# Kernel tuning notes

Hardware: AMD Instinct MI355X
Metric: run time of the kernel (lower is better)

Reference implementation:

```python
import jax, jax.numpy as jnp
import numpy as np
from jax import lax

CHANNELS, MID, GROUPS, PATCH = 512, 512, 8, 16
DROP_RATE = 0.1
NEG = -1e9


def setup_inputs() -> dict:
    key = jax.random.key(0)
    k0, k1, k2, k3, k4, k5 = jax.random.split(key, 6)
    B, T = 2, 8192
    x = jax.random.normal(k0, (B, CHANNELS, T), dtype=jnp.float32)
    # weight-norm conv is reparametrized plain conv; sample small weights directly
    W_qkv = jax.random.normal(k1, (3 * MID, CHANNELS // GROUPS, 5, 1), dtype=jnp.float32) * 0.05
    b_qkv = jax.random.normal(k2, (3 * MID,), dtype=jnp.float32) * 0.05
    W_out = jax.random.normal(k3, (CHANNELS, MID, 3), dtype=jnp.float32) * 0.05
    b_out = jax.random.normal(k4, (CHANNELS,), dtype=jnp.float32) * 0.05
    # bernoulli(p=dropRate) mask on k (detached in the original), shape of k
    drop_mask = (jax.random.uniform(k5, (B, MID, T // PATCH, PATCH)) < DROP_RATE).astype(jnp.float32)
    return {"x": x, "W_qkv": W_qkv, "b_qkv": b_qkv, "W_out": W_out, "b_out": b_out, "drop_mask": drop_mask}


def reference(x, W_qkv, b_qkv, W_out, b_out, drop_mask):
    B, C, T = x.shape
    pad = (-T) % PATCH  # static
    if pad:
        x = jnp.pad(x, ((0, 0), (0, 0), (0, pad)))
    wordNum = (T + pad) // PATCH
    x4 = x.reshape(B, C, wordNum, PATCH)  # [B,C,wordNum,patch]
    qkv = lax.conv_general_dilated(
        x4, W_qkv, window_strides=(1, 1), padding=[(2, 2), (0, 0)],
        dimension_numbers=("NCHW", "OIHW", "NCHW"), feature_group_count=GROUPS,
    ) + b_qkv[None, :, None, None]
    q, k, v = jnp.split(qkv, 3, axis=1)  # each [B,MID,wordNum,patch]
    k = k + drop_mask * NEG  # inline bernoulli dropout on k (mask is a constant)
    d = MID * PATCH

    def flat(t):  # [B,MID,wordNum,patch] -> [B,wordNum,MID*patch]
        return t.transpose(0, 2, 1, 3).reshape(B, wordNum, d)

    q = jax.nn.softmax(flat(q), axis=-1)   # softmax over features
    k = jax.nn.softmax(flat(k), axis=-2)   # softmax over sequence
    v = flat(v)
    kv = jnp.einsum("bki,bkj->bij", k, v)  # [B,d,d]
    out = jnp.einsum("bik,bkj->bij", q, kv)  # [B,wordNum,d]
    out = out.reshape(B, wordNum, MID, PATCH).transpose(0, 2, 1, 3).reshape(B, MID, wordNum * PATCH)
    out = lax.conv_general_dilated(
        out, W_out, window_strides=(1,), padding=[(1, 1)],
        dimension_numbers=("NCH", "OIH", "NCH"),
    ) + b_out[None, :, None]
    if pad:
        out = out[:, :, :-pad]
    return out
```

## Files before the change

kernel.cpp:

```cpp
#include <hip/hip_runtime.h>

#define TT 8192
#define NEGC -1000000000.0f

typedef _Float16 f16;
typedef f16 half8 __attribute__((ext_vector_type(8)));
typedef float floatx16 __attribute__((ext_vector_type(16)));

#define MFMA(a, b, c) __builtin_amdgcn_mfma_f32_32x32x16_f16(a, b, c, 0, 0, 0)

__device__ __forceinline__ half8 lds_read_frag(const f16* lds, int row, int chunk) {
    return *(const half8*)(lds + row * 64 + ((chunk ^ (row & 7)) << 3));
}
__device__ __forceinline__ void lds_write_chunk(f16* lds, int row, int chunk, half8 v) {
    *(half8*)(lds + row * 64 + ((chunk ^ (row & 7)) << 3)) = v;
}

__global__ __launch_bounds__(256) void prep_w(
    const float* __restrict__ Wq, const float* __restrict__ Wo,
    f16* __restrict__ WqP, f16* __restrict__ WoP)
{
    int i = blockIdx.x * 256 + threadIdx.x;
    const int NQ = 48 * 5 * 4 * 512;
    if (i < NQ) {
        int idx = i & 511, l = idx >> 3, e = idx & 7;
        int fi = i >> 9;
        int ks = fi & 3; fi >>= 2;
        int kh = fi % 5; int cb = fi / 5;
        int o = cb * 32 + (l & 31);
        int ci = ks * 16 + (l >> 5) * 8 + e;
        WqP[i] = (f16)Wq[o * 320 + ci * 5 + kh];
    } else {
        int j = i - NQ;
        if (j < 16 * 3 * 8 * 4 * 512) {
            int idx = j & 511, l = idx >> 3, e = idx & 7;
            int fj = j >> 9;
            int ks = fj & 3; fj >>= 2;
            int kc = fj & 7; fj >>= 3;
            int kt = fj % 3; int cb = fj / 3;
            int co = cb * 32 + (l & 31);
            int ci = kc * 64 + ks * 16 + (l >> 5) * 8 + e;
            WoP[j] = (f16)Wo[co * 1536 + ci * 3 + kt];
        }
    }
}

__global__ __launch_bounds__(256) void transpose_cvt(
    const float* __restrict__ src, size_t bstride, f16* __restrict__ dst)
{
    __shared__ float tl[64][65];
    int tid = threadIdx.x;
    int t0 = blockIdx.x * 64, c0 = blockIdx.y * 64, b = blockIdx.z;
    const float* sp = src + (size_t)b * bstride + (size_t)c0 * TT + t0;
#pragma unroll
    for (int i = 0; i < 16; i++) {
        int row = (tid >> 6) + i * 4;
        tl[row][tid & 63] = sp[(size_t)row * TT + (tid & 63)];
    }
    __syncthreads();
    f16* dp = dst + ((size_t)b * TT + t0) * 512 + c0;
#pragma unroll
    for (int i = 0; i < 16; i++) {
        int t = (tid >> 6) + i * 4;
        dp[(size_t)t * 512 + (tid & 63)] = (f16)tl[tid & 63][t];
    }
}

__global__ __launch_bounds__(256) void qkv_mfma(
    const f16* __restrict__ xT, const f16* __restrict__ WqP, const float* __restrict__ bq,
    f16* __restrict__ qk16, f16* __restrict__ vb16)
{
    __shared__ f16 xs[320 * 64];
    int tid = threadIdx.x;
    int b = blockIdx.x >> 5;
    int t0 = (blockIdx.x & 31) * 256;
    int m = blockIdx.y;
    int ob = m * 64;
    int g = m / 3;

    const f16* xb = xT + ((size_t)b * TT) * 512 + g * 64;
#pragma unroll
    for (int lp = 0; lp < 10; lp++) {
        int q = tid + lp * 256;
        int row = q >> 3, c16 = q & 7;
        int t = t0 - 32 + row;
        half8 v = {};
        if ((unsigned)t < (unsigned)TT) v = *(const half8*)(xb + (size_t)t * 512 + c16 * 8);
        lds_write_chunk(xs, row, c16, v);
    }
    __syncthreads();

    int wid = tid >> 6, l = tid & 63;
    int ln31 = l & 31, lhi = l >> 5;
    floatx16 acc[2][2] = {};
#pragma unroll
    for (int kh = 0; kh < 5; kh++) {
#pragma unroll
        for (int ks = 0; ks < 4; ks++) {
            int fi = ((m * 2) * 5 + kh) * 4 + ks;
            half8 a0 = *(const half8*)(WqP + (size_t)fi * 512 + l * 8);
            half8 a1 = *(const half8*)(WqP + (size_t)(fi + 20) * 512 + l * 8);
            int chunk = ks * 2 + lhi;
            int r0 = wid * 64 + kh * 16 + ln31;
            half8 b0 = lds_read_frag(xs, r0, chunk);
            half8 b1 = lds_read_frag(xs, r0 + 32, chunk);
            acc[0][0] = MFMA(a0, b0, acc[0][0]);
            acc[0][1] = MFMA(a0, b1, acc[0][1]);
            acc[1][0] = MFMA(a1, b0, acc[1][0]);
            acc[1][1] = MFMA(a1, b1, acc[1][1]);
        }
    }
#pragma unroll
    for (int mf = 0; mf < 2; mf++)
#pragma unroll
        for (int nf = 0; nf < 2; nf++)
#pragma unroll
            for (int r = 0; r < 16; r++) {
                int o = ob + mf * 32 + (r & 3) + 8 * (r >> 2) + 4 * lhi;
                int t = t0 + wid * 64 + nf * 32 + ln31;
                float val = acc[mf][nf][r] + bq[o];
                if (o < 1024)
                    qk16[((size_t)b * 1024 + o) * TT + t] = (f16)val;
                else
                    vb16[((size_t)b * 512 + (o - 1024)) * TT + t] = (f16)val;
            }
}

__global__ __launch_bounds__(256) void softmax_q(f16* __restrict__ qk16)
{
    int w = blockIdx.x, b = blockIdx.y, tid = threadIdx.x;
    f16* base = qk16 + (size_t)b * 1024 * TT + (size_t)w * 16;

    float val[32];
    float mx = -1e30f;
#pragma unroll
    for (int kk = 0; kk < 32; kk++) {
        int e = tid + kk * 256;
        float v = (float)base[((size_t)(e >> 4)) * TT + (e & 15)];
        val[kk] = v;
        mx = fmaxf(mx, v);
    }
#pragma unroll
    for (int o = 32; o > 0; o >>= 1) mx = fmaxf(mx, __shfl_xor(mx, o));
    __shared__ float red[4];
    int wv = tid >> 6;
    if ((tid & 63) == 0) red[wv] = mx;
    __syncthreads();
    mx = fmaxf(fmaxf(red[0], red[1]), fmaxf(red[2], red[3]));

    float s = 0.f;
#pragma unroll
    for (int kk = 0; kk < 32; kk++) { val[kk] = __expf(val[kk] - mx); s += val[kk]; }
#pragma unroll
    for (int o = 32; o > 0; o >>= 1) s += __shfl_xor(s, o);
    __syncthreads();
    if ((tid & 63) == 0) red[wv] = s;
    __syncthreads();
    s = red[0] + red[1] + red[2] + red[3];
    float inv = 1.f / s;
#pragma unroll
    for (int kk = 0; kk < 32; kk++) {
        int e = tid + kk * 256;
        base[((size_t)(e >> 4)) * TT + (e & 15)] = (f16)(val[kk] * inv);
    }
}

__global__ __launch_bounds__(256) void softmax_k(
    f16* __restrict__ qk16, const float* __restrict__ mask)
{
    int c = blockIdx.x, b = blockIdx.y, tid = threadIdx.x;
    f16* kp = qk16 + ((size_t)(b * 1024 + 512 + c)) * TT;
    const float* mp = mask + ((size_t)(b * 512 + c)) * TT;

    float val[32];
    float mx = -1e30f;
#pragma unroll
    for (int kk = 0; kk < 32; kk++) {
        int e = tid + kk * 256;
        float v = (float)kp[e] + mp[e] * NEGC;
        val[kk] = v;
        mx = fmaxf(mx, v);
    }
    mx = fmaxf(mx, __shfl_xor(mx, 16));
    mx = fmaxf(mx, __shfl_xor(mx, 32));
    __shared__ float red[4][16];
    int wv = tid >> 6, ln = tid & 63;
    if (ln < 16) red[wv][ln] = mx;
    __syncthreads();
    int p = tid & 15;
    mx = fmaxf(fmaxf(red[0][p], red[1][p]), fmaxf(red[2][p], red[3][p]));

    float s = 0.f;
#pragma unroll
    for (int kk = 0; kk < 32; kk++) { val[kk] = __expf(val[kk] - mx); s += val[kk]; }
    s += __shfl_xor(s, 16);
    s += __shfl_xor(s, 32);
    __syncthreads();
    if (ln < 16) red[wv][ln] = s;
    __syncthreads();
    s = red[0][p] + red[1][p] + red[2][p] + red[3][p];
    float inv = 1.f / s;
#pragma unroll
    for (int kk = 0; kk < 32; kk++)
        kp[tid + kk * 256] = (f16)(val[kk] * inv);
}

__global__ __launch_bounds__(256) void vperm(
    const f16* __restrict__ vb16, f16* __restrict__ vpw)
{
    int c = blockIdx.x, b = blockIdx.y, tid = threadIdx.x;
    __shared__ f16 tl[512 * 17];
    const f16* ip = vb16 + ((size_t)b * 512 + c) * TT;
    f16* op = vpw + ((size_t)b * 512 + c) * 16 * 512;
#pragma unroll
    for (int i = 0; i < 32; i++) {
        int e = tid + i * 256;
        tl[(e >> 4) * 17 + (e & 15)] = ip[e];
    }
    __syncthreads();
#pragma unroll
    for (int i = 0; i < 32; i++) {
        int o = tid + i * 256;
        op[o] = tl[(o & 511) * 17 + (o >> 9)];
    }
}

__global__ __launch_bounds__(256) void qk_mfma(
    const f16* __restrict__ qk16, float* __restrict__ Spart)
{
    __shared__ f16 As[128 * 64];
    __shared__ f16 Bs[128 * 64];
    int tid = threadIdx.x;
    int mt = blockIdx.x & 3, nt = blockIdx.x >> 2;
    int kz = blockIdx.y, b = blockIdx.z;
    int iw0 = mt * 128, w0 = nt * 128;
    const f16* qb_ = qk16 + (size_t)b * 1024 * TT;
    const f16* kb_ = qb_ + (size_t)512 * TT;
    int wid = tid >> 6, l = tid & 63, ln31 = l & 31, lhi = l >> 5;
    int wm = (wid >> 1) * 64, wn = (wid & 1) * 64;
    floatx16 acc[2][2] = {};

    for (int step = 0; step < 8; step++) {
        int c_abs = kz * 32 + step * 4 + wid;
        __syncthreads();
        const f16* qrow = qb_ + (size_t)c_abs * TT + iw0 * 16;
        const f16* krow = kb_ + (size_t)c_abs * TT + w0 * 16;
#pragma unroll
        for (int i = 0; i < 4; i++) {
            int j = l + i * 64;
            int row = j >> 1, ch = wid * 2 + (j & 1);
            lds_write_chunk(As, row, ch, *(const half8*)(qrow + j * 8));
            lds_write_chunk(Bs, row, ch, *(const half8*)(krow + j * 8));
        }
        __syncthreads();
#pragma unroll
        for (int ks = 0; ks < 4; ks++) {
            int chunk = ks * 2 + lhi;
            half8 a0 = lds_read_frag(As, wm + ln31, chunk);
            half8 a1 = lds_read_frag(As, wm + 32 + ln31, chunk);
            half8 b0 = lds_read_frag(Bs, wn + ln31, chunk);
            half8 b1 = lds_read_frag(Bs, wn + 32 + ln31, chunk);
            acc[0][0] = MFMA(a0, b0, acc[0][0]);
            acc[0][1] = MFMA(a0, b1, acc[0][1]);
            acc[1][0] = MFMA(a1, b0, acc[1][0]);
            acc[1][1] = MFMA(a1, b1, acc[1][1]);
        }
    }
    float* Sp = Spart + ((size_t)(kz * 2 + b) * 512) * 512;
#pragma unroll
    for (int mf = 0; mf < 2; mf++)
#pragma unroll
        for (int nf = 0; nf < 2; nf++)
#pragma unroll
            for (int r = 0; r < 16; r++) {
                int iw = iw0 + wm + mf * 32 + (r & 3) + 8 * (r >> 2) + 4 * lhi;
                int w = w0 + wn + nf * 32 + ln31;
                Sp[(size_t)iw * 512 + w] = acc[mf][nf][r];
            }
}

__global__ __launch_bounds__(256) void s_reduce(
    const float* __restrict__ Spart, f16* __restrict__ S16)
{
    int id = blockIdx.x * 256 + threadIdx.x;
    float s = 0.f;
#pragma unroll
    for (int kz = 0; kz < 16; kz++) s += Spart[(size_t)kz * 524288 + id];
    S16[id] = (f16)s;
}

__global__ __launch_bounds__(256) void sv_mfma(
    const f16* __restrict__ S16, const f16* __restrict__ vpw, f16* __restrict__ abufT)
{
    __shared__ f16 As[128 * 64];
    __shared__ f16 Bs[128 * 64];
    int tid = threadIdx.x;
    int mt = blockIdx.x, nt = blockIdx.y;
    int b = blockIdx.z >> 4, p = blockIdx.z & 15;
    int iw0 = mt * 128, c0n = nt * 128;
    const f16* Sb = S16 + (size_t)b * 512 * 512;
    const f16* vb_ = vpw + ((size_t)b * 512) * 16 * 512;
    int wid = tid >> 6, l = tid & 63, ln31 = l & 31, lhi = l >> 5;
    int wm = (wid >> 1) * 64, wn = (wid & 1) * 64;
    floatx16 acc[2][2] = {};

    for (int step = 0; step < 8; step++) {
        int w0k = step * 64;
        __syncthreads();
#pragma unroll
        for (int li = 0; li < 4; li++) {
            int q = tid + li * 256;
            int row = q >> 3, c16 = q & 7;
            half8 av = *(const half8*)(Sb + (size_t)(iw0 + row) * 512 + w0k + c16 * 8);
            half8 bv = *(const half8*)(vb_ + ((size_t)(c0n + row) * 16 + p) * 512 + w0k + c16 * 8);
            lds_write_chunk(As, row, c16, av);
            lds_write_chunk(Bs, row, c16, bv);
        }
        __syncthreads();
#pragma unroll
        for (int ks = 0; ks < 4; ks++) {
            int chunk = ks * 2 + lhi;
            half8 a0 = lds_read_frag(As, wm + ln31, chunk);
            half8 a1 = lds_read_frag(As, wm + 32 + ln31, chunk);
            half8 b0 = lds_read_frag(Bs, wn + ln31, chunk);
            half8 b1 = lds_read_frag(Bs, wn + 32 + ln31, chunk);
            acc[0][0] = MFMA(a0, b0, acc[0][0]);
            acc[0][1] = MFMA(a0, b1, acc[0][1]);
            acc[1][0] = MFMA(a1, b0, acc[1][0]);
            acc[1][1] = MFMA(a1, b1, acc[1][1]);
        }
    }
#pragma unroll
    for (int mf = 0; mf < 2; mf++)
#pragma unroll
        for (int nf = 0; nf < 2; nf++)
#pragma unroll
            for (int r = 0; r < 16; r++) {
                int iw = iw0 + wm + mf * 32 + (r & 3) + 8 * (r >> 2) + 4 * lhi;
                int c = c0n + wn + nf * 32 + ln31;
                int t = iw * 16 + p;
                abufT[((size_t)b * TT + t) * 512 + c] = (f16)acc[mf][nf][r];
            }
}

__global__ __launch_bounds__(256) void out_mfma(
    const f16* __restrict__ abufT, const f16* __restrict__ WoP, const float* __restrict__ bo,
    float* __restrict__ out)
{
    __shared__ f16 Bs[130 * 64];
    int tid = threadIdx.x;
    int b = blockIdx.x >> 6;
    int t0 = (blockIdx.x & 63) * 128;
    int co0 = blockIdx.y * 128;
    const f16* ab = abufT + ((size_t)b * TT) * 512;
    int wid = tid >> 6, l = tid & 63, ln31 = l & 31, lhi = l >> 5;
    int wm = (wid >> 1) * 64, wn = (wid & 1) * 64;
    int cb0 = blockIdx.y * 4 + (wid >> 1) * 2;
    floatx16 acc[2][2] = {};

    for (int kc = 0; kc < 8; kc++) {
        int ci0 = kc * 64;
        __syncthreads();
#pragma unroll
        for (int li = 0; li < 5; li++) {
            int q = tid + li * 256;
            if (q < 1040) {
                int row = q >> 3, c16 = q & 7;
                int t = t0 - 1 + row;
                half8 v = {};
                if ((unsigned)t < (unsigned)TT) v = *(const half8*)(ab + (size_t)t * 512 + ci0 + c16 * 8);
                lds_write_chunk(Bs, row, c16, v);
            }
        }
        __syncthreads();
#pragma unroll
        for (int kt = 0; kt < 3; kt++) {
#pragma unroll
            for (int ks = 0; ks < 4; ks++) {
                int fi = ((cb0 * 3 + kt) * 8 + kc) * 4 + ks;
                half8 a0 = *(const half8*)(WoP + (size_t)fi * 512 + l * 8);
                half8 a1 = *(const half8*)(WoP + (size_t)(fi + 96) * 512 + l * 8);
                int chunk = ks * 2 + lhi;
                int r0 = wn + ln31 + kt;
                half8 b0 = lds_read_frag(Bs, r0, chunk);
                half8 b1 = lds_read_frag(Bs, r0 + 32, chunk);
                acc[0][0] = MFMA(a0, b0, acc[0][0]);
                acc[0][1] = MFMA(a0, b1, acc[0][1]);
                acc[1][0] = MFMA(a1, b0, acc[1][0]);
                acc[1][1] = MFMA(a1, b1, acc[1][1]);
            }
        }
    }
#pragma unroll
    for (int mf = 0; mf < 2; mf++)
#pragma unroll
        for (int nf = 0; nf < 2; nf++)
#pragma unroll
            for (int r = 0; r < 16; r++) {
                int co = co0 + wm + mf * 32 + (r & 3) + 8 * (r >> 2) + 4 * lhi;
                int t = t0 + wn + nf * 32 + ln31;
                out[((size_t)b * 512 + co) * TT + t] = acc[mf][nf][r] + bo[co];
            }
}

extern "C" void kernel_launch(void* const* d_in, const int* in_sizes, int n_in,
                              void* d_out, int out_size, void* d_ws, size_t ws_size,
                              hipStream_t stream)
{
    const float* x    = (const float*)d_in[0];
    const float* Wq   = (const float*)d_in[1];
    const float* bq   = (const float*)d_in[2];
    const float* Wo   = (const float*)d_in[3];
    const float* bo   = (const float*)d_in[4];
    const float* mask = (const float*)d_in[5];
    float* out = (float*)d_out;
    (void)in_sizes; (void)n_in; (void)out_size; (void)ws_size;

    char* W = (char*)d_ws;
    f16*   qk16  = (f16*)W;
    f16*   xT    = (f16*)(W + 33554432);
    f16*   abufT = xT;
    f16*   vb16  = (f16*)(W + 50331648);
    f16*   vpw   = (f16*)(W + 67108864);
    float* Spart = (float*)(W + 83886080);
    f16*   S16   = (f16*)(W + 117440512);
    f16*   WqP   = (f16*)(W + 118489088);
    f16*   WoP   = (f16*)(W + 119472128);

    prep_w<<<4992, 256, 0, stream>>>(Wq, Wo, WqP, WoP);
    transpose_cvt<<<dim3(128, 8, 2), 256, 0, stream>>>(x, (size_t)512 * TT, xT);
    qkv_mfma<<<dim3(64, 24), 256, 0, stream>>>(xT, WqP, bq, qk16, vb16);
    softmax_q<<<dim3(512, 2), 256, 0, stream>>>(qk16);
    softmax_k<<<dim3(512, 2), 256, 0, stream>>>(qk16, mask);
    vperm<<<dim3(512, 2), 256, 0, stream>>>(vb16, vpw);
    qk_mfma<<<dim3(16, 16, 2), 256, 0, stream>>>(qk16, Spart);
    s_reduce<<<2048, 256, 0, stream>>>(Spart, S16);
    sv_mfma<<<dim3(4, 4, 32), 256, 0, stream>>>(S16, vpw, abufT);
    out_mfma<<<dim3(128, 4), 256, 0, stream>>>(abufT, WoP, bo, out);
}
```

Before: 286.9 us.

## Retile qkv and output convs, rewrite q-softmax with online reduction, store partials in fp16

The qkv conv kernel now computes all 192 output channels of a group per block, reusing one LDS B-fragment across six MFMAs so the input is loaded once per group instead of three times. The output conv uses the same pattern with four channel fragments per B read. softmax_q is rewritten as a 1024-thread online-softmax that reads coalesced along t rather than gathering across channels. Split-K partials for S are now stored in fp16 and reduced with vectorized loads, halving that traffic at some cost in accumulation precision.

After: 283.1 us. Within noise of the previous version (-1.3%).

```diff
diff --git a/kernel.cpp b/kernel.cpp
--- a/kernel.cpp
+++ b/kernel.cpp
@@ -70,17 +70,15 @@
     const f16* __restrict__ xT, const f16* __restrict__ WqP, const float* __restrict__ bq,
     f16* __restrict__ qk16, f16* __restrict__ vb16)
 {
-    __shared__ f16 xs[320 * 64];
-    int tid = threadIdx.x;
-    int b = blockIdx.x >> 5;
-    int t0 = (blockIdx.x & 31) * 256;
-    int m = blockIdx.y;
-    int ob = m * 64;
-    int g = m / 3;
+    __shared__ f16 xs[192 * 64];
+    int tid = threadIdx.x;
+    int b = blockIdx.x >> 6;
+    int t0 = (blockIdx.x & 63) * 128;
+    int g = blockIdx.y;
 
     const f16* xb = xT + ((size_t)b * TT) * 512 + g * 64;
 #pragma unroll
-    for (int lp = 0; lp < 10; lp++) {
+    for (int lp = 0; lp < 6; lp++) {
         int q = tid + lp * 256;
         int row = q >> 3, c16 = q & 7;
         int t = t0 - 32 + row;
@@ -92,76 +90,82 @@
 
     int wid = tid >> 6, l = tid & 63;
     int ln31 = l & 31, lhi = l >> 5;
-    floatx16 acc[2][2] = {};
+    floatx16 acc[6] = {};
 #pragma unroll
     for (int kh = 0; kh < 5; kh++) {
 #pragma unroll
         for (int ks = 0; ks < 4; ks++) {
-            int fi = ((m * 2) * 5 + kh) * 4 + ks;
-            half8 a0 = *(const half8*)(WqP + (size_t)fi * 512 + l * 8);
-            half8 a1 = *(const half8*)(WqP + (size_t)(fi + 20) * 512 + l * 8);
             int chunk = ks * 2 + lhi;
-            int r0 = wid * 64 + kh * 16 + ln31;
-            half8 b0 = lds_read_frag(xs, r0, chunk);
-            half8 b1 = lds_read_frag(xs, r0 + 32, chunk);
-            acc[0][0] = MFMA(a0, b0, acc[0][0]);
-            acc[0][1] = MFMA(a0, b1, acc[0][1]);
-            acc[1][0] = MFMA(a1, b0, acc[1][0]);
-            acc[1][1] = MFMA(a1, b1, acc[1][1]);
-        }
-    }
-#pragma unroll
-    for (int mf = 0; mf < 2; mf++)
-#pragma unroll
-        for (int nf = 0; nf < 2; nf++)
-#pragma unroll
-            for (int r = 0; r < 16; r++) {
-                int o = ob + mf * 32 + (r & 3) + 8 * (r >> 2) + 4 * lhi;
-                int t = t0 + wid * 64 + nf * 32 + ln31;
-                float val = acc[mf][nf][r] + bq[o];
-                if (o < 1024)
-                    qk16[((size_t)b * 1024 + o) * TT + t] = (f16)val;
-                else
-                    vb16[((size_t)b * 512 + (o - 1024)) * TT + t] = (f16)val;
+            half8 bfrag = lds_read_frag(xs, wid * 32 + kh * 16 + ln31, chunk);
+#pragma unroll
+            for (int cf = 0; cf < 6; cf++) {
+                int fi = ((g * 6 + cf) * 5 + kh) * 4 + ks;
+                half8 a = *(const half8*)(WqP + (size_t)fi * 512 + l * 8);
+                acc[cf] = MFMA(a, bfrag, acc[cf]);
             }
-}
-
-__global__ __launch_bounds__(256) void softmax_q(f16* __restrict__ qk16)
-{
-    int w = blockIdx.x, b = blockIdx.y, tid = threadIdx.x;
-    f16* base = qk16 + (size_t)b * 1024 * TT + (size_t)w * 16;
-
-    float val[32];
-    float mx = -1e30f;
-#pragma unroll
-    for (int kk = 0; kk < 32; kk++) {
-        int e = tid + kk * 256;
-        float v = (float)base[((size_t)(e >> 4)) * TT + (e & 15)];
-        val[kk] = v;
-        mx = fmaxf(mx, v);
-    }
-#pragma unroll
-    for (int o = 32; o > 0; o >>= 1) mx = fmaxf(mx, __shfl_xor(mx, o));
-    __shared__ float red[4];
-    int wv = tid >> 6;
-    if ((tid & 63) == 0) red[wv] = mx;
-    __syncthreads();
-    mx = fmaxf(fmaxf(red[0], red[1]), fmaxf(red[2], red[3]));
-
-    float s = 0.f;
-#pragma unroll
-    for (int kk = 0; kk < 32; kk++) { val[kk] = __expf(val[kk] - mx); s += val[kk]; }
-#pragma unroll
-    for (int o = 32; o > 0; o >>= 1) s += __shfl_xor(s, o);
-    __syncthreads();
-    if ((tid & 63) == 0) red[wv] = s;
-    __syncthreads();
-    s = red[0] + red[1] + red[2] + red[3];
-    float inv = 1.f / s;
-#pragma unroll
-    for (int kk = 0; kk < 32; kk++) {
-        int e = tid + kk * 256;
-        base[((size_t)(e >> 4)) * TT + (e & 15)] = (f16)(val[kk] * inv);
+        }
+    }
+    int t = t0 + wid * 32 + ln31;
+#pragma unroll
+    for (int cf = 0; cf < 6; cf++)
+#pragma unroll
+        for (int r = 0; r < 16; r++) {
+            int o = g * 192 + cf * 32 + (r & 3) + 8 * (r >> 2) + 4 * lhi;
+            float val = acc[cf][r] + bq[o];
+            if (o < 1024)
+                qk16[((size_t)b * 1024 + o) * TT + t] = (f16)val;
+            else
+                vb16[((size_t)b * 512 + (o - 1024)) * TT + t] = (f16)val;
+        }
+}
+
+__global__ __launch_bounds__(1024) void softmax_q(f16* __restrict__ qk16)
+{
+    __shared__ float redm[16][64], reds[16][64];
+    __shared__ float colM[64], colS[64];
+    int tid = threadIdx.x;
+    int lt = tid & 63, strip = tid >> 6;
+    int b = blockIdx.y;
+    f16* base = qk16 + (size_t)b * 1024 * TT + blockIdx.x * 64 + lt;
+
+    float m = -1e30f, s = 0.f;
+#pragma unroll 4
+    for (int cc = 0; cc < 32; cc++) {
+        int c = strip * 32 + cc;
+        float v = (float)base[(size_t)c * TT];
+        float nm = fmaxf(m, v);
+        s = s * __expf(m - nm) + __expf(v - nm);
+        m = nm;
+    }
+    redm[strip][lt] = m; reds[strip][lt] = s;
+    __syncthreads();
+    if (strip == 0) {
+        float M = -1e30f, S = 0.f;
+#pragma unroll
+        for (int k = 0; k < 16; k++) {
+            float mm = redm[k][lt], ss = reds[k][lt];
+            float nm = fmaxf(M, mm);
+            S = S * __expf(M - nm) + ss * __expf(mm - nm);
+            M = nm;
+        }
+        colM[lt] = M; colS[lt] = S;
+    }
+    __syncthreads();
+    float M = -1e30f, S = 0.f;
+    int w0 = lt & 48;
+#pragma unroll
+    for (int j = 0; j < 16; j++) {
+        float mm = colM[w0 + j], ss = colS[w0 + j];
+        float nm = fmaxf(M, mm);
+        S = S * __expf(M - nm) + ss * __expf(mm - nm);
+        M = nm;
+    }
+    float inv = 1.f / S;
+#pragma unroll 4
+    for (int cc = 0; cc < 32; cc++) {
+        int c = strip * 32 + cc;
+        float v = (float)base[(size_t)c * TT];
+        base[(size_t)c * TT] = (f16)(__expf(v - M) * inv);
     }
 }
 
@@ -226,7 +230,7 @@
 }
 
 __global__ __launch_bounds__(256) void qk_mfma(
-    const f16* __restrict__ qk16, float* __restrict__ Spart)
+    const f16* __restrict__ qk16, f16* __restrict__ Sp16)
 {
     __shared__ f16 As[128 * 64];
     __shared__ f16 Bs[128 * 64];
@@ -266,7 +270,7 @@
             acc[1][1] = MFMA(a1, b1, acc[1][1]);
         }
     }
-    float* Sp = Spart + ((size_t)(kz * 2 + b) * 512) * 512;
+    f16* Sp = Sp16 + ((size_t)(kz * 2 + b)) * 262144;
 #pragma unroll
     for (int mf = 0; mf < 2; mf++)
 #pragma unroll
@@ -275,18 +279,25 @@
             for (int r = 0; r < 16; r++) {
                 int iw = iw0 + wm + mf * 32 + (r & 3) + 8 * (r >> 2) + 4 * lhi;
                 int w = w0 + wn + nf * 32 + ln31;
-                Sp[(size_t)iw * 512 + w] = acc[mf][nf][r];
+                Sp[(size_t)iw * 512 + w] = (f16)acc[mf][nf][r];
             }
 }
 
 __global__ __launch_bounds__(256) void s_reduce(
-    const float* __restrict__ Spart, f16* __restrict__ S16)
+    const f16* __restrict__ Sp16, f16* __restrict__ S16)
 {
     int id = blockIdx.x * 256 + threadIdx.x;
-    float s = 0.f;
-#pragma unroll
-    for (int kz = 0; kz < 16; kz++) s += Spart[(size_t)kz * 524288 + id];
-    S16[id] = (f16)s;
+    float acc[8] = {};
+#pragma unroll
+    for (int kz = 0; kz < 16; kz++) {
+        half8 v = *(const half8*)(Sp16 + (size_t)kz * 524288 + (size_t)id * 8);
+#pragma unroll
+        for (int j = 0; j < 8; j++) acc[j] += (float)v[j];
+    }
+    half8 o;
+#pragma unroll
+    for (int j = 0; j < 8; j++) o[j] = (f16)acc[j];
+    *(half8*)(S16 + (size_t)id * 8) = o;
 }
 
 __global__ __launch_bounds__(256) void sv_mfma(
@@ -351,12 +362,10 @@
     int tid = threadIdx.x;
     int b = blockIdx.x >> 6;
     int t0 = (blockIdx.x & 63) * 128;
-    int co0 = blockIdx.y * 128;
+    int cbb = blockIdx.y;
     const f16* ab = abufT + ((size_t)b * TT) * 512;
     int wid = tid >> 6, l = tid & 63, ln31 = l & 31, lhi = l >> 5;
-    int wm = (wid >> 1) * 64, wn = (wid & 1) * 64;
-    int cb0 = blockIdx.y * 4 + (wid >> 1) * 2;
-    floatx16 acc[2][2] = {};
+    floatx16 acc[4] = {};
 
     for (int kc = 0; kc < 8; kc++) {
         int ci0 = kc * 64;
@@ -377,30 +386,25 @@
         for (int kt = 0; kt < 3; kt++) {
 #pragma unroll
             for (int ks = 0; ks < 4; ks++) {
-                int fi = ((cb0 * 3 + kt) * 8 + kc) * 4 + ks;
-                half8 a0 = *(const half8*)(WoP + (size_t)fi * 512 + l * 8);
-                half8 a1 = *(const half8*)(WoP + (size_t)(fi + 96) * 512 + l * 8);
                 int chunk = ks * 2 + lhi;
-                int r0 = wn + ln31 + kt;
-                half8 b0 = lds_read_frag(Bs, r0, chunk);
-                half8 b1 = lds_read_frag(Bs, r0 + 32, chunk);
-                acc[0][0] = MFMA(a0, b0, acc[0][0]);
-                acc[0][1] = MFMA(a0, b1, acc[0][1]);
-                acc[1][0] = MFMA(a1, b0, acc[1][0]);
-                acc[1][1] = MFMA(a1, b1, acc[1][1]);
+                half8 bfrag = lds_read_frag(Bs, wid * 32 + ln31 + kt, chunk);
+#pragma unroll
+                for (int cf = 0; cf < 4; cf++) {
+                    int fi = (((cbb * 4 + cf) * 3 + kt) * 8 + kc) * 4 + ks;
+                    half8 a = *(const half8*)(WoP + (size_t)fi * 512 + l * 8);
+                    acc[cf] = MFMA(a, bfrag, acc[cf]);
+                }
             }
         }
     }
-#pragma unroll
-    for (int mf = 0; mf < 2; mf++)
-#pragma unroll
-        for (int nf = 0; nf < 2; nf++)
-#pragma unroll
-            for (int r = 0; r < 16; r++) {
-                int co = co0 + wm + mf * 32 + (r & 3) + 8 * (r >> 2) + 4 * lhi;
-                int t = t0 + wn + nf * 32 + ln31;
-                out[((size_t)b * 512 + co) * TT + t] = acc[mf][nf][r] + bo[co];
-            }
+    int t = t0 + wid * 32 + ln31;
+#pragma unroll
+    for (int cf = 0; cf < 4; cf++)
+#pragma unroll
+        for (int r = 0; r < 16; r++) {
+            int co = cbb * 128 + cf * 32 + (r & 3) + 8 * (r >> 2) + 4 * lhi;
+            out[((size_t)b * 512 + co) * TT + t] = acc[cf][r] + bo[co];
+        }
 }
 
 extern "C" void kernel_launch(void* const* d_in, const int* in_sizes, int n_in,
@@ -422,19 +426,19 @@
     f16*   abufT = xT;
     f16*   vb16  = (f16*)(W + 50331648);
     f16*   vpw   = (f16*)(W + 67108864);
-    float* Spart = (float*)(W + 83886080);
+    f16*   Sp16  = (f16*)(W + 83886080);
     f16*   S16   = (f16*)(W + 117440512);
     f16*   WqP   = (f16*)(W + 118489088);
     f16*   WoP   = (f16*)(W + 119472128);
 
     prep_w<<<4992, 256, 0, stream>>>(Wq, Wo, WqP, WoP);
     transpose_cvt<<<dim3(128, 8, 2), 256, 0, stream>>>(x, (size_t)512 * TT, xT);
-    qkv_mfma<<<dim3(64, 24), 256, 0, stream>>>(xT, WqP, bq, qk16, vb16);
-    softmax_q<<<dim3(512, 2), 256, 0, stream>>>(qk16);
+    qkv_mfma<<<dim3(128, 8), 256, 0, stream>>>(xT, WqP, bq, qk16, vb16);
+    softmax_q<<<dim3(128, 2), 1024, 0, stream>>>(qk16);
     softmax_k<<<dim3(512, 2), 256, 0, stream>>>(qk16, mask);
     vperm<<<dim3(512, 2), 256, 0, stream>>>(vb16, vpw);
-    qk_mfma<<<dim3(16, 16, 2), 256, 0, stream>>>(qk16, Spart);
-    s_reduce<<<2048, 256, 0, stream>>>(Spart, S16);
+    qk_mfma<<<dim3(16, 16, 2), 256, 0, stream>>>(qk16, Sp16);
+    s_reduce<<<256, 256, 0, stream>>>(Sp16, S16);
     sv_mfma<<<dim3(4, 4, 32), 256, 0, stream>>>(S16, vpw, abufT);
     out_mfma<<<dim3(128, 4), 256, 0, stream>>>(abufT, WoP, bo, out);
 }
```
